# Optimization experiments

Measured on AMD Instinct MI355X. Metric: run time of the kernel, lower is better.

The kernel has to match this reference:

```python
import jax, jax.numpy as jnp
import numpy as np

N = 20000      # nodes
E = 80000      # edges (before self loops)
NG = 64        # graphs in batch
EMB = 780      # embedding_size (768 text + 12 time)
NEG_SLOPE = 0.2
BN_EPS = 1e-5


def setup_inputs() -> dict:
    key = jax.random.key(0)
    ks = jax.random.split(key, 20)
    def rn(k, shape, s=0.05):
        return jax.random.normal(k, shape, dtype=jnp.float32) * s
    z = lambda n: jnp.zeros((n,), dtype=jnp.float32)
    o = lambda n: jnp.ones((n,), dtype=jnp.float32)
    x = jax.random.normal(ks[0], (N, 772), dtype=jnp.float32)
    edge_index = jax.random.randint(ks[1], (2, E), 0, N)
    batch = jnp.sort(jax.random.randint(ks[2], (N,), 0, NG))
    return dict(
        x=x, edge_index=edge_index, batch=batch,
        time_W=rn(ks[3], (4, 12)), time_b=z(12),
        lin_W0=rn(ks[4], (EMB, 3 * EMB)), att_src0=rn(ks[5], (3, EMB)), att_dst0=rn(ks[6], (3, EMB)),
        bias0=z(3 * EMB), gamma0=o(3 * EMB), beta0=z(3 * EMB),
        lin_W1=rn(ks[7], (3 * EMB, 3 * EMB)), att_src1=rn(ks[8], (3, EMB)), att_dst1=rn(ks[9], (3, EMB)),
        bias1=z(3 * EMB), gamma1=o(3 * EMB), beta1=z(3 * EMB),
        lin_W2=rn(ks[10], (3 * EMB, EMB)), att_src2=rn(ks[11], (1, EMB)), att_dst2=rn(ks[12], (1, EMB)),
        bias2=z(EMB), gamma2=o(EMB), beta2=z(EMB),
        mlp_W1=rn(ks[13], (EMB, 128)), mlp_b1=z(128),
        mlp_W2=rn(ks[14], (128, 64)), mlp_b2=z(64),
    )


def _gat_layer(h, src, dst, W, a_src, a_dst, b, heads):
    # PyG GATConv (eval mode: dropout off), concat=True, self loops already in src/dst
    C = W.shape[1] // heads
    hp = (h @ W).reshape(N, heads, C)                       # [N,H,C]
    a_s = jnp.sum(hp * a_src[None], axis=-1)                # [N,H]
    a_d = jnp.sum(hp * a_dst[None], axis=-1)                # [N,H]
    e = jax.nn.leaky_relu(a_s[src] + a_d[dst], NEG_SLOPE)   # [E+N,H]
    m = jax.ops.segment_max(e, dst, num_segments=N)         # segment softmax over incoming edges
    m = jnp.where(jnp.isfinite(m), m, 0.0)
    p = jnp.exp(e - m[dst])
    denom = jax.ops.segment_sum(p, dst, num_segments=N)
    alpha = p / (denom[dst] + 1e-16)                        # [E+N,H]
    out = jax.ops.segment_sum(alpha[:, :, None] * hp[src], dst, num_segments=N)  # [N,H,C]
    return out.reshape(N, heads * C) + b


def _bn(h, gamma, beta):
    # BatchNorm in training-mode math (batch statistics, biased variance)
    mu = jnp.mean(h, axis=0)
    var = jnp.mean((h - mu) ** 2, axis=0)
    return (h - mu) * jax.lax.rsqrt(var + BN_EPS) * gamma + beta


def reference(x, edge_index, batch, time_W, time_b,
              lin_W0, att_src0, att_dst0, bias0, gamma0, beta0,
              lin_W1, att_src1, att_dst1, bias1, gamma1, beta1,
              lin_W2, att_src2, att_dst2, bias2, gamma2, beta2,
              mlp_W1, mlp_b1, mlp_W2, mlp_b2):
    te = x[:, 768:772] @ time_W + time_b
    h = jnp.concatenate([jax.lax.stop_gradient(x[:, :768]), te,
                         jax.lax.stop_gradient(x[:, 772:])], axis=-1)  # [N, 780]
    sl = jnp.arange(N)
    src = jnp.concatenate([edge_index[0], sl])   # add self loops
    dst = jnp.concatenate([edge_index[1], sl])
    layers = [
        (lin_W0, att_src0, att_dst0, bias0, gamma0, beta0, 3),
        (lin_W1, att_src1, att_dst1, bias1, gamma1, beta1, 3),
        (lin_W2, att_src2, att_dst2, bias2, gamma2, beta2, 1),
    ]
    for W, a_s, a_d, b, g, bt, heads in layers:
        h = jnp.tanh(_gat_layer(h, src, dst, W, a_s, a_d, b, heads))
        h = _bn(h, g, bt)
    cnt = jax.ops.segment_sum(jnp.ones((N,), dtype=h.dtype), batch, num_segments=NG)
    pooled = jax.ops.segment_sum(h, batch, num_segments=NG) / jnp.maximum(cnt, 1.0)[:, None]
    pooled = jax.nn.relu(pooled)
    out = jnp.tanh(pooled @ mlp_W1 + mlp_b1) @ mlp_W2 + mlp_b2
    return out  # [NG, 64]
```

## Files before the change

kernel.cpp:

```cpp
#include <hip/hip_runtime.h>
#include <math.h>

#define NN   20000
#define EE   80000
#define ELP  100000
#define NGR  64
#define EMB  780
#define W3   2340
#define EMBP 832
#define W3P  2368
#define NZ   (W3+8)

static inline int cdiv_i(long long a, long long b){ return (int)((a + b - 1) / b); }

typedef _Float16 f16;
typedef _Float16 f16x4 __attribute__((ext_vector_type(4)));
typedef _Float16 f16x8 __attribute__((ext_vector_type(8)));
typedef float    f32x4 __attribute__((ext_vector_type(4)));

__device__ __forceinline__ void async_ld16(const f16* g, f16* l){
    __builtin_amdgcn_global_load_lds(
        (const __attribute__((address_space(1))) unsigned int*)g,
        (__attribute__((address_space(3))) unsigned int*)l,
        16, 0, 0);
}

__global__ void k_zero_f32(float* p, int n){
    int i = blockIdx.x*256 + threadIdx.x; if (i < n) p[i] = 0.f;
}
__global__ void k_zero_i32(int* p, int n){
    int i = blockIdx.x*256 + threadIdx.x; if (i < n) p[i] = 0;
}

__global__ void k_transpose(const float* __restrict__ W, f16* __restrict__ Wt,
                            const float* __restrict__ sc, const float* __restrict__ sh,
                            float* __restrict__ dvec, int K, int N, int KP){
    __shared__ float T[32][33];
    __shared__ float D[8][33];
    int n0 = blockIdx.x*32, k0 = blockIdx.y*32;
    int tx = threadIdx.x, ty = threadIdx.y;
    float raw[4];
#pragma unroll
    for (int r = 0; r < 4; r++){
        int k = k0 + ty + r*8;
        float w = 0.f;
        if (k < K && n0 + tx < N) w = W[(size_t)k*N + n0 + tx];
        raw[r] = w;
        T[ty + r*8][tx] = sc ? w * ((k < K) ? sc[k] : 0.f) : w;
    }
    if (sh){
        float p = 0.f;
#pragma unroll
        for (int r = 0; r < 4; r++){
            int k = k0 + ty + r*8;
            if (k < K) p += sh[k] * raw[r];
        }
        D[ty][tx] = p;
    }
    __syncthreads();
#pragma unroll
    for (int r = 0; r < 4; r++){
        int n = n0 + ty + r*8;
        int k = k0 + tx;
        if (n < N && k < KP) Wt[(size_t)n*KP + k] = (f16)T[tx][ty + r*8];
    }
    if (sh && ty == 0 && n0 + tx < N){
        float s = 0.f;
#pragma unroll
        for (int j = 0; j < 8; j++) s += D[j][tx];
        atomicAdd(&dvec[n0 + tx], s);
    }
}

__global__ void k_wvec(const float* __restrict__ W, const float* __restrict__ asrc,
                       const float* __restrict__ adst, const float* __restrict__ sc,
                       f16* __restrict__ Wt, float* __restrict__ dvec,
                       int K, int N, int KP, int H){
    int k = blockIdx.x*4 + (threadIdx.x >> 6);
    int lane = threadIdx.x & 63;
    if (k < K){
        const float* row = W + (size_t)k*N;
        float acc[6];
#pragma unroll
        for (int i = 0; i < 6; i++) acc[i] = 0.f;
        for (int c = lane; c < EMB; c += 64){
            for (int h = 0; h < H; h++){
                float wv = row[h*EMB + c];
                acc[h]     += wv * asrc[h*EMB + c];
                acc[H + h] += wv * adst[h*EMB + c];
            }
        }
        float s = sc ? sc[k] : 1.f;
        for (int i = 0; i < 2*H; i++){
            float v = acc[i];
#pragma unroll
            for (int off = 32; off; off >>= 1) v += __shfl_xor(v, off);
            if (lane == 0) Wt[(size_t)(N + i)*KP + k] = (f16)(v * s);
        }
    }
    if (blockIdx.x == 0){
        int wv = threadIdx.x >> 6;
        for (int i = wv; i < 2*H; i += 4){
            int h = (i < H) ? i : (i - H);
            const float* att = (i < H) ? (asrc + h*EMB) : (adst + h*EMB);
            float s = 0.f;
            for (int c = lane; c < EMB; c += 64) s += dvec[h*EMB + c] * att[c];
#pragma unroll
            for (int off = 32; off; off >>= 1) s += __shfl_xor(s, off);
            if (lane == 0) dvec[N + i] = s;
        }
    }
}

__global__ void k_build_h(const float* __restrict__ x, const float* __restrict__ tW,
                          const float* __restrict__ tb, f16* __restrict__ h){
    int idx = blockIdx.x*256 + threadIdx.x;
    int total = NN*(EMBP/4);
    if (idx >= total) return;
    int n = idx / (EMBP/4);
    int c0 = (idx - n*(EMBP/4))*4;
    const float* xr = x + (size_t)n*772;
    f16x4 o;
#pragma unroll
    for (int j = 0; j < 4; j++){
        int c = c0 + j; float v;
        if (c < 768) v = xr[c];
        else if (c < EMB){
            int t = c - 768;
            v = tb[t] + xr[768]*tW[t] + xr[769]*tW[12+t] + xr[770]*tW[24+t] + xr[771]*tW[36+t];
        } else v = 0.f;
        o[j] = (f16)v;
    }
    *(f16x4*)(h + (size_t)n*EMBP + c0) = o;
}

__global__ void k_deg(const int* __restrict__ ei, int* __restrict__ deg){
    int k = blockIdx.x*256 + threadIdx.x; if (k >= ELP) return;
    int d = (k < EE) ? ei[EE + k] : (k - EE);
    atomicAdd(&deg[d], 1);
}

__global__ __launch_bounds__(1024) void k_scan(int* __restrict__ deg, int* __restrict__ rp){
    __shared__ int part[1024];
    int tid = threadIdx.x;
    int i0 = tid*20;
    int n = (i0 < NN) ? min(20, NN - i0) : 0;
    int s = 0;
    for (int k = 0; k < n; k++) s += deg[i0+k];
    part[tid] = s; __syncthreads();
    for (int off = 1; off < 1024; off <<= 1){
        int t = (tid >= off) ? part[tid-off] : 0;
        __syncthreads();
        part[tid] += t;
        __syncthreads();
    }
    int run = part[tid] - s;
    for (int k = 0; k < n; k++){
        int d = deg[i0+k];
        rp[i0+k] = run;
        deg[i0+k] = run;
        run += d;
    }
    if (tid == 1023) rp[NN] = part[1023];
}

__global__ void k_fill(const int* __restrict__ ei, int* __restrict__ cursor, int* __restrict__ csrc){
    int k = blockIdx.x*256 + threadIdx.x; if (k >= ELP) return;
    int s, d;
    if (k < EE){ s = ei[k]; d = ei[EE + k]; } else { s = k - EE; d = s; }
    int pos = atomicAdd(&cursor[d], 1);
    csrc[pos] = s;
}

__global__ void k_grp(const int* __restrict__ batch, int* __restrict__ grp){
    int g = blockIdx.x*256 + threadIdx.x; if (g > NGR) return;
    int lo = 0, hi = NN;
    while (lo < hi){ int mid = (lo+hi)>>1; if (batch[mid] < g) lo = mid+1; else hi = mid; }
    grp[g] = lo;
}

__global__ __launch_bounds__(512, 4) void k_gemmT(const f16* __restrict__ A,
                                                  const f16* __restrict__ Bt,
                                                  const float* __restrict__ dvec,
                                                  f16* __restrict__ C,
                                                  float* __restrict__ a_sd,
                                                  int M, int N, int NB, int H,
                                                  int KP, int SN, int Mtiles, int NT){
    __shared__ f16 smem[36864];
    f16* sB = smem + 12288;

    int nwg = Mtiles*NT;
    int bid = blockIdx.x;
    int q = nwg >> 3, r = nwg & 7, xcd = bid & 7, lin = bid >> 3;
    int wg = (xcd < r ? xcd*(q+1) : r*(q+1) + (xcd - r)*q) + lin;
    int mt = wg / NT, nt = wg - mt*NT;
    int m0 = mt*128, n0 = nt*256;

    int tid = threadIdx.x;
    int w = tid >> 6, lane = tid & 63;
    int lm = lane & 15, lq = lane >> 4;
    int wm = w >> 2, wn = w & 3;

    int kqs = ((lane & 3) ^ ((lane >> 3) & 3)) * 8;
    const f16* gA0 = A  + (size_t)min(m0 + w*16 + (lane >> 2), M-1)*KP + kqs;
    const f16* gB0 = Bt + (size_t)min(n0 + w*32 + (lane >> 2), NB-1)*KP + kqs;
    const f16* gB1 = Bt + (size_t)min(n0 + w*32 + 16 + (lane >> 2), NB-1)*KP + kqs;
    int sa0 = w*512;
    int sb0 = w*1024, sb1 = w*1024 + 512;

    int swz  = (lq ^ ((lm >> 1) & 3)) * 8;
    int aoff = (wm*64 + lm)*32 + swz;
    int boff = (wn*64 + lm)*32 + swz;

    f32x4 acc[4][4];
#pragma unroll
    for (int i = 0; i < 4; i++)
#pragma unroll
        for (int j = 0; j < 4; j++) acc[i][j] = (f32x4)0.f;

    int KT = KP >> 5;

    async_ld16(gA0,      &smem[sa0]);
    async_ld16(gB0,      &sB[sb0]);
    async_ld16(gB1,      &sB[sb1]);
    async_ld16(gA0 + 32, &smem[4096 + sa0]);
    async_ld16(gB0 + 32, &sB[8192 + sb0]);
    async_ld16(gB1 + 32, &sB[8192 + sb1]);
    asm volatile("s_waitcnt vmcnt(3)" ::: "memory");
    __builtin_amdgcn_s_barrier();

    int cur = 0, nx2 = 2;
    for (int t = 0; t < KT; t++){
        int ac = cur*4096, bc = cur*8192;
        f16x8 aF[4], bF[4];
#pragma unroll
        for (int i = 0; i < 4; i++) aF[i] = *(const f16x8*)&smem[ac + aoff + i*512];
#pragma unroll
        for (int i = 0; i < 4; i++) bF[i] = *(const f16x8*)&sB[bc + boff + i*512];
        bool s2 = (t+2 < KT);
        if (s2){
            int ko2 = (t+2)*32;
            int a2 = nx2*4096, b2 = nx2*8192;
            async_ld16(gA0 + ko2, &smem[a2 + sa0]);
            async_ld16(gB0 + ko2, &sB[b2 + sb0]);
            async_ld16(gB1 + ko2, &sB[b2 + sb1]);
        }
        __builtin_amdgcn_s_setprio(1);
#pragma unroll
        for (int i = 0; i < 4; i++)
#pragma unroll
            for (int j = 0; j < 4; j++)
                acc[i][j] = __builtin_amdgcn_mfma_f32_16x16x32_f16(aF[i], bF[j], acc[i][j], 0, 0, 0);
        __builtin_amdgcn_s_setprio(0);
        if (s2) asm volatile("s_waitcnt vmcnt(3)" ::: "memory");
        else    asm volatile("s_waitcnt vmcnt(0)" ::: "memory");
        __builtin_amdgcn_s_barrier();
        cur = (cur == 2) ? 0 : cur + 1;
        nx2 = (nx2 == 2) ? 0 : nx2 + 1;
    }

#pragma unroll
    for (int mi = 0; mi < 4; mi++){
#pragma unroll
        for (int ni = 0; ni < 4; ni++){
            int col = n0 + wn*64 + ni*16 + lm;
            if (col >= N && col < NB){
                int jc = col - N;
                int idx = (jc < H) ? jc : (3 + jc - H);
                float dv = dvec[col];
                int rbase = m0 + wm*64 + mi*16 + lq*4;
#pragma unroll
                for (int rr = 0; rr < 4; rr++){
                    int row = rbase + rr;
                    if (row < M) a_sd[(size_t)row*6 + idx] = acc[mi][ni][rr] + dv;
                }
            }
        }
    }

    float dv4[4];
#pragma unroll
    for (int ni = 0; ni < 4; ni++){
        int gcol = n0 + wn*64 + ni*16 + lm;
        dv4[ni] = (gcol < N) ? dvec[gcol] : 0.f;
    }
    int ncols = min(256, N - n0);
#pragma unroll
    for (int mi = 0; mi < 4; mi++){
#pragma unroll
        for (int ni = 0; ni < 4; ni++){
            int colL = wn*64 + ni*16 + lm;
#pragma unroll
            for (int rr = 0; rr < 4; rr++){
                int rowL = wm*64 + mi*16 + lq*4 + rr;
                smem[rowL*264 + colL] = (f16)(acc[mi][ni][rr] + dv4[ni]);
            }
        }
    }
    asm volatile("s_waitcnt lgkmcnt(0)" ::: "memory");
    __builtin_amdgcn_s_barrier();
#pragma unroll
    for (int it = 0; it < 8; it++){
        int ch = tid + it*512;
        int rowL = ch >> 5, cc = (ch & 31)*8;
        int grow = m0 + rowL;
        if (grow < M && cc < ncols){
            if (cc + 8 <= ncols){
                f16x8 v = *(f16x8*)&smem[rowL*264 + cc];
                *(f16x8*)(C + (size_t)grow*SN + n0 + cc) = v;
            } else {
                for (int jj = cc; jj < ncols; jj++)
                    C[(size_t)grow*SN + n0 + jj] = smem[rowL*264 + jj];
            }
        }
    }
}

__global__ __launch_bounds__(256, 3) void k_gemmS(const f16* __restrict__ A,
                                                  const f16* __restrict__ Bt,
                                                  const float* __restrict__ dvec,
                                                  f16* __restrict__ C,
                                                  float* __restrict__ a_sd,
                                                  int M, int N, int NB, int H,
                                                  int KP, int SN, int Mtiles, int NT){
    __shared__ f16 smem[24576];
    f16* sB = smem + 12288;

    int nwg = Mtiles*NT;
    int bid = blockIdx.x;
    int q = nwg >> 3, r = nwg & 7, xcd = bid & 7, lin = bid >> 3;
    int wg = (xcd < r ? xcd*(q+1) : r*(q+1) + (xcd - r)*q) + lin;
    int mt = wg / NT, nt = wg - mt*NT;
    int m0 = mt*128, n0 = nt*128;

    int tid = threadIdx.x;
    int w = tid >> 6, lane = tid & 63;
    int lm = lane & 15, lq = lane >> 4;
    int wm = w >> 1, wn = w & 1;

    int kqs = ((lane & 3) ^ ((lane >> 3) & 3)) * 8;
    const f16* gA0 = A  + (size_t)min(m0 + w*32 + (lane >> 2), M-1)*KP + kqs;
    const f16* gA1 = A  + (size_t)min(m0 + w*32 + 16 + (lane >> 2), M-1)*KP + kqs;
    const f16* gB0 = Bt + (size_t)min(n0 + w*32 + (lane >> 2), NB-1)*KP + kqs;
    const f16* gB1 = Bt + (size_t)min(n0 + w*32 + 16 + (lane >> 2), NB-1)*KP + kqs;
    int sa0 = w*1024, sa1 = w*1024 + 512;
    int sb0 = w*1024, sb1 = w*1024 + 512;

    int swz  = (lq ^ ((lm >> 1) & 3)) * 8;
    int aoff = (wm*64 + lm)*32 + swz;
    int boff = (wn*64 + lm)*32 + swz;

    f32x4 acc[4][4];
#pragma unroll
    for (int i = 0; i < 4; i++)
#pragma unroll
        for (int j = 0; j < 4; j++) acc[i][j] = (f32x4)0.f;

    int KT = KP >> 5;

    async_ld16(gA0,      &smem[sa0]);        async_ld16(gA1,      &smem[sa1]);
    async_ld16(gB0,      &sB[sb0]);          async_ld16(gB1,      &sB[sb1]);
    async_ld16(gA0 + 32, &smem[4096 + sa0]); async_ld16(gA1 + 32, &smem[4096 + sa1]);
    async_ld16(gB0 + 32, &sB[4096 + sb0]);   async_ld16(gB1 + 32, &sB[4096 + sb1]);
    asm volatile("s_waitcnt vmcnt(4)" ::: "memory");
    __builtin_amdgcn_s_barrier();

    int cur = 0, nx2 = 2;
    for (int t = 0; t < KT; t++){
        int ac = cur*4096, bc = cur*4096;
        f16x8 aF[4], bF[4];
#pragma unroll
        for (int i = 0; i < 4; i++) aF[i] = *(const f16x8*)&smem[ac + aoff + i*512];
#pragma unroll
        for (int i = 0; i < 4; i++) bF[i] = *(const f16x8*)&sB[bc + boff + i*512];
        bool s2 = (t+2 < KT);
        if (s2){
            int ko2 = (t+2)*32;
            int a2 = nx2*4096, b2 = nx2*4096;
            async_ld16(gA0 + ko2, &smem[a2 + sa0]); async_ld16(gA1 + ko2, &smem[a2 + sa1]);
            async_ld16(gB0 + ko2, &sB[b2 + sb0]);   async_ld16(gB1 + ko2, &sB[b2 + sb1]);
        }
        __builtin_amdgcn_s_setprio(1);
#pragma unroll
        for (int i = 0; i < 4; i++)
#pragma unroll
            for (int j = 0; j < 4; j++)
                acc[i][j] = __builtin_amdgcn_mfma_f32_16x16x32_f16(aF[i], bF[j], acc[i][j], 0, 0, 0);
        __builtin_amdgcn_s_setprio(0);
        if (s2) asm volatile("s_waitcnt vmcnt(4)" ::: "memory");
        else    asm volatile("s_waitcnt vmcnt(0)" ::: "memory");
        __builtin_amdgcn_s_barrier();
        cur = (cur == 2) ? 0 : cur + 1;
        nx2 = (nx2 == 2) ? 0 : nx2 + 1;
    }

#pragma unroll
    for (int mi = 0; mi < 4; mi++){
#pragma unroll
        for (int ni = 0; ni < 4; ni++){
            int col = n0 + wn*64 + ni*16 + lm;
            if (col >= N && col < NB){
                int jc = col - N;
                int idx = (jc < H) ? jc : (3 + jc - H);
                float dv = dvec[col];
                int rbase = m0 + wm*64 + mi*16 + lq*4;
#pragma unroll
                for (int rr = 0; rr < 4; rr++){
                    int row = rbase + rr;
                    if (row < M) a_sd[(size_t)row*6 + idx] = acc[mi][ni][rr] + dv;
                }
            }
        }
    }

    float dv4[4];
#pragma unroll
    for (int ni = 0; ni < 4; ni++){
        int gcol = n0 + wn*64 + ni*16 + lm;
        dv4[ni] = (gcol < N) ? dvec[gcol] : 0.f;
    }
    int ncols = min(128, N - n0);
#pragma unroll
    for (int mi = 0; mi < 4; mi++){
#pragma unroll
        for (int ni = 0; ni < 4; ni++){
            int colL = wn*64 + ni*16 + lm;
#pragma unroll
            for (int rr = 0; rr < 4; rr++){
                int rowL = wm*64 + mi*16 + lq*4 + rr;
                smem[rowL*136 + colL] = (f16)(acc[mi][ni][rr] + dv4[ni]);
            }
        }
    }
    asm volatile("s_waitcnt lgkmcnt(0)" ::: "memory");
    __builtin_amdgcn_s_barrier();
#pragma unroll
    for (int it = 0; it < 8; it++){
        int ch = tid + it*256;
        int rowL = ch >> 4, cc = (ch & 15)*8;
        int grow = m0 + rowL;
        if (grow < M && cc < ncols){
            if (cc + 8 <= ncols){
                f16x8 v = *(f16x8*)&smem[rowL*136 + cc];
                *(f16x8*)(C + (size_t)grow*SN + n0 + cc) = v;
            } else {
                for (int jj = cc; jj < ncols; jj++)
                    C[(size_t)grow*SN + n0 + jj] = smem[rowL*136 + jj];
            }
        }
    }
}

template<int H>
__global__ __launch_bounds__(256) void k_alpha(const int* __restrict__ rp, const int* __restrict__ csrc,
                                               const float* __restrict__ a_sd, float* __restrict__ alpha){
    int n = blockIdx.x*4 + (threadIdx.x >> 6);
    if (n >= NN) return;
    int lane = threadIdx.x & 63;
    int beg = rp[n], deg = rp[n+1] - beg;

    float adv[H];
#pragma unroll
    for (int h = 0; h < H; h++) adv[h] = a_sd[(size_t)n*6 + 3 + h];

    bool act0 = lane < deg;
    int sl0 = 0; float t0[H];
    if (act0){
        sl0 = csrc[beg + lane];
#pragma unroll
        for (int h = 0; h < H; h++){
            float t = a_sd[(size_t)sl0*6 + h] + adv[h];
            t0[h] = t > 0.f ? t : 0.2f*t;
        }
    } else {
#pragma unroll
        for (int h = 0; h < H; h++) t0[h] = -1e30f;
    }

    float mx[H];
#pragma unroll
    for (int h = 0; h < H; h++) mx[h] = t0[h];
    for (int base = 64; base < deg; base += 64){
        int e = base + lane;
        if (e < deg){
            int s = csrc[beg + e];
#pragma unroll
            for (int h = 0; h < H; h++){
                float t = a_sd[(size_t)s*6 + h] + adv[h];
                t = t > 0.f ? t : 0.2f*t;
                mx[h] = fmaxf(mx[h], t);
            }
        }
    }
#pragma unroll
    for (int off = 32; off; off >>= 1)
#pragma unroll
        for (int h = 0; h < H; h++) mx[h] = fmaxf(mx[h], __shfl_xor(mx[h], off));

    float dn[H];
#pragma unroll
    for (int h = 0; h < H; h++) dn[h] = act0 ? expf(t0[h] - mx[h]) : 0.f;
    for (int base = 64; base < deg; base += 64){
        int e = base + lane;
        if (e < deg){
            int s = csrc[beg + e];
#pragma unroll
            for (int h = 0; h < H; h++){
                float t = a_sd[(size_t)s*6 + h] + adv[h];
                t = t > 0.f ? t : 0.2f*t;
                dn[h] += expf(t - mx[h]);
            }
        }
    }
#pragma unroll
    for (int off = 32; off; off >>= 1)
#pragma unroll
        for (int h = 0; h < H; h++) dn[h] += __shfl_xor(dn[h], off);
    float inv[H];
#pragma unroll
    for (int h = 0; h < H; h++) inv[h] = 1.f / (dn[h] + 1e-16f);

    if (act0){
        if (H == 3){
            float4 o;
            o.x = expf(t0[0]-mx[0])*inv[0];
            o.y = expf(t0[1]-mx[1])*inv[1];
            o.z = expf(t0[2]-mx[2])*inv[2];
            o.w = 0.f;
            *(float4*)(alpha + (size_t)(beg+lane)*4) = o;
        } else {
            alpha[beg+lane] = expf(t0[0]-mx[0])*inv[0];
        }
    }
    for (int base = 64; base < deg; base += 64){
        int e = base + lane;
        if (e < deg){
            int s = csrc[beg + e];
            float av[H];
#pragma unroll
            for (int h = 0; h < H; h++){
                float t = a_sd[(size_t)s*6 + h] + adv[h];
                t = t > 0.f ? t : 0.2f*t;
                av[h] = expf(t - mx[h]) * inv[h];
            }
            if (H == 3){
                float4 o; o.x = av[0]; o.y = av[1]; o.z = av[2]; o.w = 0.f;
                *(float4*)(alpha + (size_t)(beg+e)*4) = o;
            } else {
                alpha[beg+e] = av[0];
            }
        }
    }
}

template<int H>
__global__ __launch_bounds__(256) void k_gather(const f16* __restrict__ hp, const int* __restrict__ rp,
                                                const int* __restrict__ csrc, const float* __restrict__ alpha,
                                                const float* __restrict__ bias, f16* __restrict__ y,
                                                int SP, int W){
    int w = threadIdx.x >> 6, lane = threadIdx.x & 63;
    int n = blockIdx.x*4 + w;
    if (n >= NN) return;
    int c = blockIdx.y*512 + lane*8;
    bool cok = c < SP;
    int beg = rp[n], deg = rp[n+1] - beg;

    int hl = 0, hh = 0, nsp = 8;
    if (H == 3){
        hl = min(c/EMB, 2); hh = min((c+7)/EMB, 2);
        nsp = (hh > hl) ? (EMB*(hl+1) - c) : 8;
    }
    float acc[8];
#pragma unroll
    for (int j = 0; j < 8; j++) acc[j] = 0.f;

    for (int base = 0; base < deg; base += 64){
        int cnt = min(64, deg - base);
        int e0 = base + lane;
        int sl = 0; float a0v = 0.f, a1v = 0.f, a2v = 0.f;
        if (e0 < deg){
            sl = csrc[beg + e0];
            if (H == 3){
                float4 al4 = *(const float4*)(alpha + (size_t)(beg+e0)*4);
                a0v = al4.x; a1v = al4.y; a2v = al4.z;
            } else {
                a0v = alpha[beg + e0];
            }
        }
#pragma unroll 4
        for (int e = 0; e < cnt; e++){
            int s = __shfl(sl, e);
            float b0 = __shfl(a0v, e);
            float b1 = (H==3) ? __shfl(a1v, e) : b0;
            float b2 = (H==3) ? __shfl(a2v, e) : b0;
            if (cok){
                f16x8 v = *(const f16x8*)(hp + (size_t)s*SP + c);
                float lo = (H==3) ? ((hl==0)?b0:((hl==1)?b1:b2)) : b0;
                float hi = (H==3) ? ((hh==0)?b0:((hh==1)?b1:b2)) : b0;
#pragma unroll
                for (int j = 0; j < 8; j++)
                    acc[j] += ((j < nsp) ? lo : hi) * (float)v[j];
            }
        }
    }

    if (cok){
        f16x8 o;
#pragma unroll
        for (int j = 0; j < 8; j++){
            float vv = (c + j < W) ? tanhf(acc[j] + bias[c+j]) : 0.f;
            o[j] = (f16)vv;
        }
        *(f16x8*)(y + (size_t)n*SP + c) = o;
    }
}

__global__ void k_bnstat(const f16* __restrict__ y, float* __restrict__ ps,
                         float* __restrict__ pq, int W, int SP){
    int c0 = (blockIdx.x*256 + threadIdx.x)*4;
    if (c0 >= W) return;
    int slice = blockIdx.y;
    int r0 = (int)(((long long)NN*slice)/128);
    int r1 = (int)(((long long)NN*(slice+1))/128);
    float s[4] = {0,0,0,0}, q[4] = {0,0,0,0};
    for (int r = r0; r < r1; r++){
        f16x4 u = *(const f16x4*)(y + (size_t)r*SP + c0);
#pragma unroll
        for (int j = 0; j < 4; j++){ float v = (float)u[j]; s[j] += v; q[j] += v*v; }
    }
#pragma unroll
    for (int j = 0; j < 4; j++){
        ps[(size_t)slice*W3 + c0+j] = s[j];
        pq[(size_t)slice*W3 + c0+j] = q[j];
    }
}

__global__ void k_bnfin(const float* __restrict__ ps, const float* __restrict__ pq,
                        const float* __restrict__ gamma, const float* __restrict__ beta,
                        float* __restrict__ sc, float* __restrict__ sh,
                        float* __restrict__ dvec, int W, int zn){
    int c = blockIdx.x*256 + threadIdx.x;
    if (c < W){
        float m = 0.f, q = 0.f;
        for (int s = 0; s < 128; s++){ m += ps[(size_t)s*W3 + c]; q += pq[(size_t)s*W3 + c]; }
        m *= (1.f/NN);
        float v = q * (1.f/NN) - m*m;
        float is = 1.f / sqrtf(v + 1e-5f);
        float g = gamma[c];
        sc[c] = is * g;
        sh[c] = beta[c] - m * is * g;
    }
    if (c < zn) dvec[c] = 0.f;
}

__global__ void k_pool(const f16* __restrict__ h, const int* __restrict__ grp,
                       float* __restrict__ pooled){
    int g = blockIdx.x;
    int c = threadIdx.x*4;
    if (c >= EMB) return;
    int r0 = grp[g], r1 = grp[g+1];
    float s0=0.f, s1=0.f, s2=0.f, s3=0.f;
    for (int r = r0; r < r1; r++){
        f16x4 u = *(const f16x4*)(h + (size_t)r*EMBP + c);
        s0 += (float)u[0]; s1 += (float)u[1]; s2 += (float)u[2]; s3 += (float)u[3];
    }
    pooled[g*EMB + c] = s0; pooled[g*EMB + c+1] = s1;
    pooled[g*EMB + c+2] = s2; pooled[g*EMB + c+3] = s3;
}

__global__ __launch_bounds__(256) void k_mlp(const float* __restrict__ pooled, const int* __restrict__ grp,
                                             const float* __restrict__ sc, const float* __restrict__ sh,
                                             const float* __restrict__ W1, const float* __restrict__ b1,
                                             const float* __restrict__ W2, const float* __restrict__ b2,
                                             float* __restrict__ out){
    __shared__ float p[EMB];
    __shared__ float hid[128];
    int g = blockIdx.x, tid = threadIdx.x;
    int cnt = grp[g+1] - grp[g];
    float ic = 1.f / fmaxf((float)cnt, 1.f);
    for (int c = tid; c < EMB; c += 256){
        float v = pooled[g*EMB + c] * ic * sc[c] + sh[c];
        p[c] = v > 0.f ? v : 0.f;
    }
    __syncthreads();
    if (tid < 128){
        float s = b1[tid];
        for (int k = 0; k < EMB; k++) s += p[k] * W1[k*128 + tid];
        hid[tid] = tanhf(s);
    }
    __syncthreads();
    if (tid < 64){
        float s = b2[tid];
        for (int k = 0; k < 128; k++) s += hid[k] * W2[k*64 + tid];
        out[g*64 + tid] = s;
    }
}

extern "C" void kernel_launch(void* const* d_in, const int* in_sizes, int n_in,
                              void* d_out, int out_size, void* d_ws, size_t ws_size,
                              hipStream_t stream) {
    (void)in_sizes; (void)n_in; (void)out_size;
    const float* x    = (const float*)d_in[0];
    const int*   ei   = (const int*)  d_in[1];
    const int*   batch= (const int*)  d_in[2];
    const float* tW   = (const float*)d_in[3];
    const float* tb   = (const float*)d_in[4];
    const float* W0   = (const float*)d_in[5];
    const float* as0  = (const float*)d_in[6];
    const float* ad0  = (const float*)d_in[7];
    const float* b0   = (const float*)d_in[8];
    const float* g0   = (const float*)d_in[9];
    const float* be0  = (const float*)d_in[10];
    const float* W1   = (const float*)d_in[11];
    const float* as1  = (const float*)d_in[12];
    const float* ad1  = (const float*)d_in[13];
    const float* b1   = (const float*)d_in[14];
    const float* g1   = (const float*)d_in[15];
    const float* be1  = (const float*)d_in[16];
    const float* W2   = (const float*)d_in[17];
    const float* as2  = (const float*)d_in[18];
    const float* ad2  = (const float*)d_in[19];
    const float* b2   = (const float*)d_in[20];
    const float* g2   = (const float*)d_in[21];
    const float* be2  = (const float*)d_in[22];
    const float* mW1  = (const float*)d_in[23];
    const float* mb1  = (const float*)d_in[24];
    const float* mW2  = (const float*)d_in[25];
    const float* mb2  = (const float*)d_in[26];
    float* outp = (float*)d_out;

    size_t off = 0;
    auto carve = [&](size_t bytes) -> void* {
        void* p = (char*)d_ws + off;
        off = (off + bytes + 255) & ~(size_t)255;
        return p;
    };
    f16* big1 = (f16*)carve((size_t)NN*W3P*2);
    f16* big2 = (f16*)carve((size_t)NN*W3P*2);
    f16* Wt   = (f16*)carve((size_t)NZ*W3P*2);
    float* a_sd  = (float*)carve((size_t)NN*6*4);
    float* psum  = (float*)carve((size_t)128*W3*4);
    float* psq   = (float*)carve((size_t)128*W3*4);
    float* sc    = (float*)carve((size_t)W3*4);
    float* sh    = (float*)carve((size_t)W3*4);
    float* dvec  = (float*)carve((size_t)NZ*4);
    float* alphab= (float*)carve((size_t)ELP*4*4);
    float* pooled= (float*)carve((size_t)NGR*EMB*4);
    int*   grp   = (int*)carve((size_t)(NGR+1)*4);
    int*   deg   = (int*)carve((size_t)NN*4);
    int*   rp    = (int*)carve((size_t)(NN+1)*4);
    int*   csrc  = (int*)carve((size_t)ELP*4);

    if (ws_size < off) return;

    k_zero_i32<<<cdiv_i(NN,256),256,0,stream>>>(deg, NN);
    k_deg<<<cdiv_i(ELP,256),256,0,stream>>>(ei, deg);
    k_scan<<<1,1024,0,stream>>>(deg, rp);
    k_fill<<<cdiv_i(ELP,256),256,0,stream>>>(ei, deg, csrc);
    k_grp<<<1,256,0,stream>>>(batch, grp);

    k_build_h<<<cdiv_i((long long)NN*(EMBP/4),256),256,0,stream>>>(x, tW, tb, big1);
    k_zero_f32<<<cdiv_i(NZ,256),256,0,stream>>>(dvec, NZ);

    struct Layer { const float* W; const float* as; const float* ad; const float* b;
                   const float* g; const float* be; int H; int K; int KP; };
    Layer layers[3] = {
        {W0, as0, ad0, b0, g0, be0, 3, EMB, EMBP},
        {W1, as1, ad1, b1, g1, be1, 3, W3,  W3P },
        {W2, as2, ad2, b2, g2, be2, 1, W3,  W3P },
    };

    for (int L = 0; L < 3; L++){
        Layer& ly = layers[L];
        int Wout  = ly.H * EMB;
        int NB    = Wout + 2*ly.H;
        int SPout = (Wout == W3) ? W3P : EMBP;
        const float* scale = (L == 0) ? nullptr : sc;
        const float* shift = (L == 0) ? nullptr : sh;

        dim3 tg(cdiv_i(Wout,32), cdiv_i(ly.KP,32));
        k_transpose<<<tg, dim3(32,8), 0, stream>>>(ly.W, Wt, scale, shift, dvec, ly.K, Wout, ly.KP);
        k_wvec<<<cdiv_i(ly.K,4),256,0,stream>>>(ly.W, ly.as, ly.ad, scale, Wt, dvec, ly.K, Wout, ly.KP, ly.H);

        if (L < 2){
            int Mtiles = cdiv_i(NN,128), NT = cdiv_i(NB,256);
            k_gemmT<<<Mtiles*NT, 512, 0, stream>>>(big1, Wt, dvec, big2, a_sd,
                                                   NN, Wout, NB, ly.H, ly.KP, SPout, Mtiles, NT);
        } else {
            int Mtiles = cdiv_i(NN,128), NT = cdiv_i(NB,128);
            k_gemmS<<<Mtiles*NT, 256, 0, stream>>>(big1, Wt, dvec, big2, a_sd,
                                                   NN, Wout, NB, ly.H, ly.KP, SPout, Mtiles, NT);
        }

        dim3 gg(cdiv_i(NN,4), cdiv_i(SPout,512));
        if (ly.H == 3){
            k_alpha<3><<<cdiv_i(NN,4),256,0,stream>>>(rp, csrc, a_sd, alphab);
            k_gather<3><<<gg,256,0,stream>>>(big2, rp, csrc, alphab, ly.b, big1, SPout, Wout);
        } else {
            k_alpha<1><<<cdiv_i(NN,4),256,0,stream>>>(rp, csrc, a_sd, alphab);
            k_gather<1><<<gg,256,0,stream>>>(big2, rp, csrc, alphab, ly.b, big1, SPout, Wout);
        }

        dim3 gs(cdiv_i(Wout/4,256), 128);
        k_bnstat<<<gs,256,0,stream>>>(big1, psum, psq, Wout, SPout);
        int zn = (L < 2) ? NZ : 0;
        k_bnfin<<<cdiv_i(Wout,256),256,0,stream>>>(psum, psq, ly.g, ly.be, sc, sh, dvec, Wout, zn);
    }

    k_pool<<<NGR,256,0,stream>>>(big1, grp, pooled);
    k_mlp<<<NGR,256,0,stream>>>(pooled, grp, sc, sh, mW1, mb1, mW2, mb2, outp);
}
```

Before: 1.398 ms.

## Aggregate before projecting in layer 0 using per-head grouped GEMM

For the first GAT layer, attention logits are computed directly from the 780-wide input through precomputed attention weight vectors. Neighbour features are then aggregated per head in the narrow input space, and a per-head GEMM projects the aggregated features with bias and tanh fused into its epilogue. This exploits linearity, (sum alpha*h)W equals sum alpha*(hW), so the gather reads 780-wide rows instead of 2340-wide rows. The price is three GEMMs on 800-wide K, one per head, and an extra pass to zero the padding columns. The workspace layout is reordered so the aggregation buffer can reuse big2.

```diff
diff --git a/kernel.cpp b/kernel.cpp
--- a/kernel.cpp
+++ b/kernel.cpp
@@ -10,6 +10,7 @@
 #define EMBP 832
 #define W3P  2368
 #define NZ   (W3+8)
+#define KPA  800
 
 static inline int cdiv_i(long long a, long long b){ return (int)((a + b - 1) / b); }
 
@@ -30,6 +31,13 @@
 }
 __global__ void k_zero_i32(int* p, int n){
     int i = blockIdx.x*256 + threadIdx.x; if (i < n) p[i] = 0;
+}
+__global__ void k_padzero(f16* y){
+    int i = blockIdx.x*256 + threadIdx.x;
+    if (i >= NN*7) return;
+    int rw = i / 7, c = W3 + (i - rw*7)*4;
+    f16x4 z; z[0]=(f16)0.f; z[1]=(f16)0.f; z[2]=(f16)0.f; z[3]=(f16)0.f;
+    *(f16x4*)(y + (size_t)rw*W3P + c) = z;
 }
 
 __global__ void k_transpose(const float* __restrict__ W, f16* __restrict__ Wt,
@@ -447,6 +455,219 @@
                 for (int jj = cc; jj < ncols; jj++)
                     C[(size_t)grow*SN + n0 + jj] = smem[rowL*136 + jj];
             }
+        }
+    }
+}
+
+__global__ __launch_bounds__(256, 3) void k_gemmH(const f16* __restrict__ A,
+                                                  const f16* __restrict__ Bt,
+                                                  const float* __restrict__ bias,
+                                                  f16* __restrict__ Y,
+                                                  int Mtiles, int NT){
+    const int KPB = 832, Mh = NN, Nh = 780, KT = KPA >> 5;
+    __shared__ f16 smem[24576];
+    f16* sB = smem + 12288;
+
+    int nwg = 3*Mtiles*NT;
+    int bid = blockIdx.x;
+    int q = nwg >> 3, r = nwg & 7, xcd = bid & 7, lin = bid >> 3;
+    int wg = (xcd < r ? xcd*(q+1) : r*(q+1) + (xcd - r)*q) + lin;
+    int hd = wg / (Mtiles*NT);
+    int rem = wg - hd*(Mtiles*NT);
+    int mt = rem / NT, nt = rem - mt*NT;
+    int m0 = mt*128, n0 = nt*128;
+    const f16* Ah = A  + (size_t)hd*NN*KPA;
+    const f16* Bh = Bt + (size_t)hd*Nh*KPB;
+
+    int tid = threadIdx.x;
+    int w = tid >> 6, lane = tid & 63;
+    int lm = lane & 15, lq = lane >> 4;
+    int wm = w >> 1, wn = w & 1;
+
+    int kqs = ((lane & 3) ^ ((lane >> 3) & 3)) * 8;
+    const f16* gA0 = Ah + (size_t)min(m0 + w*32 + (lane >> 2), Mh-1)*KPA + kqs;
+    const f16* gA1 = Ah + (size_t)min(m0 + w*32 + 16 + (lane >> 2), Mh-1)*KPA + kqs;
+    const f16* gB0 = Bh + (size_t)min(n0 + w*32 + (lane >> 2), Nh-1)*KPB + kqs;
+    const f16* gB1 = Bh + (size_t)min(n0 + w*32 + 16 + (lane >> 2), Nh-1)*KPB + kqs;
+    int sa0 = w*1024, sa1 = w*1024 + 512;
+
+    int swz  = (lq ^ ((lm >> 1) & 3)) * 8;
+    int aoff = (wm*64 + lm)*32 + swz;
+    int boff = (wn*64 + lm)*32 + swz;
+
+    f32x4 acc[4][4];
+#pragma unroll
+    for (int i = 0; i < 4; i++)
+#pragma unroll
+        for (int j = 0; j < 4; j++) acc[i][j] = (f32x4)0.f;
+
+    async_ld16(gA0,      &smem[sa0]);        async_ld16(gA1,      &smem[sa1]);
+    async_ld16(gB0,      &sB[sa0]);          async_ld16(gB1,      &sB[sa1]);
+    async_ld16(gA0 + 32, &smem[4096 + sa0]); async_ld16(gA1 + 32, &smem[4096 + sa1]);
+    async_ld16(gB0 + 32, &sB[4096 + sa0]);   async_ld16(gB1 + 32, &sB[4096 + sa1]);
+    asm volatile("s_waitcnt vmcnt(4)" ::: "memory");
+    __builtin_amdgcn_s_barrier();
+
+    int cur = 0, nx2 = 2;
+    for (int t = 0; t < KT; t++){
+        int ac = cur*4096;
+        f16x8 aF[4], bF[4];
+#pragma unroll
+        for (int i = 0; i < 4; i++) aF[i] = *(const f16x8*)&smem[ac + aoff + i*512];
+#pragma unroll
+        for (int i = 0; i < 4; i++) bF[i] = *(const f16x8*)&sB[ac + boff + i*512];
+        bool s2 = (t+2 < KT);
+        if (s2){
+            int ko2 = (t+2)*32;
+            int a2 = nx2*4096;
+            async_ld16(gA0 + ko2, &smem[a2 + sa0]); async_ld16(gA1 + ko2, &smem[a2 + sa1]);
+            async_ld16(gB0 + ko2, &sB[a2 + sa0]);   async_ld16(gB1 + ko2, &sB[a2 + sa1]);
+        }
+        __builtin_amdgcn_s_setprio(1);
+#pragma unroll
+        for (int i = 0; i < 4; i++)
+#pragma unroll
+            for (int j = 0; j < 4; j++)
+                acc[i][j] = __builtin_amdgcn_mfma_f32_16x16x32_f16(aF[i], bF[j], acc[i][j], 0, 0, 0);
+        __builtin_amdgcn_s_setprio(0);
+        if (s2) asm volatile("s_waitcnt vmcnt(4)" ::: "memory");
+        else    asm volatile("s_waitcnt vmcnt(0)" ::: "memory");
+        __builtin_amdgcn_s_barrier();
+        cur = (cur == 2) ? 0 : cur + 1;
+        nx2 = (nx2 == 2) ? 0 : nx2 + 1;
+    }
+
+    float bv[4];
+#pragma unroll
+    for (int ni = 0; ni < 4; ni++){
+        int col = n0 + wn*64 + ni*16 + lm;
+        bv[ni] = (col < Nh) ? bias[hd*Nh + col] : 0.f;
+    }
+    int ncols = min(128, Nh - n0);
+#pragma unroll
+    for (int mi = 0; mi < 4; mi++){
+#pragma unroll
+        for (int ni = 0; ni < 4; ni++){
+            int colL = wn*64 + ni*16 + lm;
+#pragma unroll
+            for (int rr = 0; rr < 4; rr++){
+                int rowL = wm*64 + mi*16 + lq*4 + rr;
+                smem[rowL*136 + colL] = (f16)tanhf(acc[mi][ni][rr] + bv[ni]);
+            }
+        }
+    }
+    asm volatile("s_waitcnt lgkmcnt(0)" ::: "memory");
+    __builtin_amdgcn_s_barrier();
+#pragma unroll
+    for (int it = 0; it < 8; it++){
+        int ch = tid + it*256;
+        int rowL = ch >> 4, cc = (ch & 15)*8;
+        int grow = m0 + rowL;
+        if (grow < Mh && cc < ncols){
+            size_t gb = (size_t)grow*W3P + hd*Nh + n0 + cc;
+            if (cc + 8 <= ncols){
+                *(f16x4*)(Y + gb)     = *(f16x4*)&smem[rowL*136 + cc];
+                *(f16x4*)(Y + gb + 4) = *(f16x4*)&smem[rowL*136 + cc + 4];
+            } else {
+                for (int jj = cc; jj < ncols; jj++)
+                    Y[(size_t)grow*W3P + hd*Nh + n0 + jj] = smem[rowL*136 + jj];
+            }
+        }
+    }
+}
+
+template<int H>
+__global__ __launch_bounds__(256) void k_asd(const f16* __restrict__ h, const f16* __restrict__ watt,
+                                             const float* __restrict__ dvN, float* __restrict__ a_sd,
+                                             int KP){
+    int n = blockIdx.x*4 + (threadIdx.x >> 6);
+    if (n >= NN) return;
+    int lane = threadIdx.x & 63;
+    const f16* hr = h + (size_t)n*KP;
+    float acc[2*H];
+#pragma unroll
+    for (int i = 0; i < 2*H; i++) acc[i] = 0.f;
+    for (int k0 = 0; k0 < KP; k0 += 64){
+        float hv = (float)hr[k0 + lane];
+#pragma unroll
+        for (int i = 0; i < 2*H; i++)
+            acc[i] += hv * (float)watt[(size_t)i*KP + k0 + lane];
+    }
+#pragma unroll
+    for (int off = 32; off; off >>= 1)
+#pragma unroll
+        for (int i = 0; i < 2*H; i++) acc[i] += __shfl_xor(acc[i], off);
+    if (lane == 0){
+#pragma unroll
+        for (int i = 0; i < 2*H; i++){
+            int idx = (i < H) ? i : (3 + i - H);
+            a_sd[(size_t)n*6 + idx] = acc[i] + dvN[i];
+        }
+    }
+}
+
+__global__ __launch_bounds__(256) void k_gagg(const f16* __restrict__ h, const int* __restrict__ rp,
+                                              const int* __restrict__ csrc, const float* __restrict__ alpha,
+                                              f16* __restrict__ agg){
+    int w = threadIdx.x >> 6, lane = threadIdx.x & 63;
+    int n = blockIdx.x*4 + w;
+    if (n >= NN) return;
+    int beg = rp[n], deg = rp[n+1] - beg;
+    int c0 = lane*8, c1 = 512 + lane*8;
+    bool ok1 = c1 < KPA;
+
+    float acc[3][2][8];
+#pragma unroll
+    for (int hd = 0; hd < 3; hd++)
+#pragma unroll
+        for (int g = 0; g < 2; g++)
+#pragma unroll
+            for (int j = 0; j < 8; j++) acc[hd][g][j] = 0.f;
+
+    for (int base = 0; base < deg; base += 64){
+        int cnt = min(64, deg - base);
+        int e0 = base + lane;
+        int sl = 0; float a0v = 0.f, a1v = 0.f, a2v = 0.f;
+        if (e0 < deg){
+            sl = csrc[beg + e0];
+            float4 q4 = *(const float4*)(alpha + (size_t)(beg+e0)*4);
+            a0v = q4.x; a1v = q4.y; a2v = q4.z;
+        }
+#pragma unroll 4
+        for (int e = 0; e < cnt; e++){
+            int s = __shfl(sl, e);
+            float b0 = __shfl(a0v, e);
+            float b1 = __shfl(a1v, e);
+            float b2 = __shfl(a2v, e);
+            const f16* row = h + (size_t)s*EMBP;
+            f16x8 v0 = *(const f16x8*)(row + c0);
+#pragma unroll
+            for (int j = 0; j < 8; j++){
+                float vv = (float)v0[j];
+                acc[0][0][j] += b0*vv; acc[1][0][j] += b1*vv; acc[2][0][j] += b2*vv;
+            }
+            if (ok1){
+                f16x8 v1 = *(const f16x8*)(row + c1);
+#pragma unroll
+                for (int j = 0; j < 8; j++){
+                    float vv = (float)v1[j];
+                    acc[0][1][j] += b0*vv; acc[1][1][j] += b1*vv; acc[2][1][j] += b2*vv;
+                }
+            }
+        }
+    }
+
+#pragma unroll
+    for (int hd = 0; hd < 3; hd++){
+        f16x8 o;
+#pragma unroll
+        for (int j = 0; j < 8; j++) o[j] = (f16)acc[hd][0][j];
+        *(f16x8*)(agg + ((size_t)hd*NN + n)*KPA + c0) = o;
+        if (ok1){
+            f16x8 o1;
+#pragma unroll
+            for (int j = 0; j < 8; j++) o1[j] = (f16)acc[hd][1][j];
+            *(f16x8*)(agg + ((size_t)hd*NN + n)*KPA + c1) = o1;
         }
     }
 }
@@ -737,10 +958,10 @@
     };
     f16* big1 = (f16*)carve((size_t)NN*W3P*2);
     f16* big2 = (f16*)carve((size_t)NN*W3P*2);
+    float* psum  = (float*)carve((size_t)128*W3*4);
+    float* psq   = (float*)carve((size_t)128*W3*4);
     f16* Wt   = (f16*)carve((size_t)NZ*W3P*2);
     float* a_sd  = (float*)carve((size_t)NN*6*4);
-    float* psum  = (float*)carve((size_t)128*W3*4);
-    float* psq   = (float*)carve((size_t)128*W3*4);
     float* sc    = (float*)carve((size_t)W3*4);
     float* sh    = (float*)carve((size_t)W3*4);
     float* dvec  = (float*)carve((size_t)NZ*4);
@@ -753,6 +974,8 @@
 
     if (ws_size < off) return;
 
+    f16* agg = big2;
+
     k_zero_i32<<<cdiv_i(NN,256),256,0,stream>>>(deg, NN);
     k_deg<<<cdiv_i(ELP,256),256,0,stream>>>(ei, deg);
     k_scan<<<1,1024,0,stream>>>(deg, rp);
@@ -782,23 +1005,31 @@
         k_transpose<<<tg, dim3(32,8), 0, stream>>>(ly.W, Wt, scale, shift, dvec, ly.K, Wout, ly.KP);
         k_wvec<<<cdiv_i(ly.K,4),256,0,stream>>>(ly.W, ly.as, ly.ad, scale, Wt, dvec, ly.K, Wout, ly.KP, ly.H);
 
-        if (L < 2){
-            int Mtiles = cdiv_i(NN,128), NT = cdiv_i(NB,256);
-            k_gemmT<<<Mtiles*NT, 512, 0, stream>>>(big1, Wt, dvec, big2, a_sd,
-                                                   NN, Wout, NB, ly.H, ly.KP, SPout, Mtiles, NT);
+        if (L == 0){
+            k_asd<3><<<cdiv_i(NN,4),256,0,stream>>>(big1, Wt + (size_t)Wout*ly.KP, dvec + Wout, a_sd, ly.KP);
+            k_alpha<3><<<cdiv_i(NN,4),256,0,stream>>>(rp, csrc, a_sd, alphab);
+            k_gagg<<<cdiv_i(NN,4),256,0,stream>>>(big1, rp, csrc, alphab, agg);
+            int Mtiles = cdiv_i(NN,128), NTh = cdiv_i(780,128);
+            k_gemmH<<<3*Mtiles*NTh, 256, 0, stream>>>(agg, Wt, ly.b, big1, Mtiles, NTh);
+            k_padzero<<<cdiv_i(NN*7,256),256,0,stream>>>(big1);
         } else {
-            int Mtiles = cdiv_i(NN,128), NT = cdiv_i(NB,128);
-            k_gemmS<<<Mtiles*NT, 256, 0, stream>>>(big1, Wt, dvec, big2, a_sd,
-                                                   NN, Wout, NB, ly.H, ly.KP, SPout, Mtiles, NT);
-        }
-
-        dim3 gg(cdiv_i(NN,4), cdiv_i(SPout,512));
-        if (ly.H == 3){
-            k_alpha<3><<<cdiv_i(NN,4),256,0,stream>>>(rp, csrc, a_sd, alphab);
-            k_gather<3><<<gg,256,0,stream>>>(big2, rp, csrc, alphab, ly.b, big1, SPout, Wout);
-        } else {
-            k_alpha<1><<<cdiv_i(NN,4),256,0,stream>>>(rp, csrc, a_sd, alphab);
-            k_gather<1><<<gg,256,0,stream>>>(big2, rp, csrc, alphab, ly.b, big1, SPout, Wout);
+            if (L == 1){
+                int Mtiles = cdiv_i(NN,128), NT = cdiv_i(NB,256);
+                k_gemmT<<<Mtiles*NT, 512, 0, stream>>>(big1, Wt, dvec, big2, a_sd,
+                                                       NN, Wout, NB, ly.H, ly.KP, SPout, Mtiles, NT);
+            } else {
+                int Mtiles = cdiv_i(NN,128), NT = cdiv_i(NB,128);
+                k_gemmS<<<Mtiles*NT, 256, 0, stream>>>(big1, Wt, dvec, big2, a_sd,
+                                                       NN, Wout, NB, ly.H, ly.KP, SPout, Mtiles, NT);
+            }
+            dim3 gg(cdiv_i(NN,4), cdiv_i(SPout,512));
+            if (ly.H == 3){
+                k_alpha<3><<<cdiv_i(NN,4),256,0,stream>>>(rp, csrc, a_sd, alphab);
+                k_gather<3><<<gg,256,0,stream>>>(big2, rp, csrc, alphab, ly.b, big1, SPout, Wout);
+            } else {
+                k_alpha<1><<<cdiv_i(NN,4),256,0,stream>>>(rp, csrc, a_sd, alphab);
+                k_gather<1><<<gg,256,0,stream>>>(big2, rp, csrc, alphab, ly.b, big1, SPout, Wout);
+            }
         }
 
         dim3 gs(cdiv_i(Wout/4,256), 128);
```

Result: no change. 1.382 ms (-1.1%).
